# Performance work log

Measured on AMD Instinct MI355X. Metric: run time of the kernel, lower is better.

## Reference

```python
import jax, jax.numpy as jnp
import numpy as np

NEG_SLOPE_GAT = 0.2   # PyG GATConv default negative_slope
NEG_SLOPE = 0.01      # torch.nn.LeakyReLU default
NUM_AISLES = 20       # aisle_nrs drawn from [0,20); matches aisle_nrs.max()+1


def leaky(x, s):
    return jnp.where(x >= 0, x, s * x)


def gat_conv(x, src, dst, W, a_src, a_dst, b, n_nodes):
    """Single-head PyG GATConv (self-loops already appended to src/dst)."""
    h = x @ W                                        # [N, C]
    es = h @ a_src                                   # [N]
    ed = h @ a_dst                                   # [N]
    e = leaky(es[src] + ed[dst], NEG_SLOPE_GAT)      # [E] per-edge score
    m = jax.ops.segment_max(e, dst, num_segments=n_nodes)
    w = jnp.exp(e - m[dst])
    z = jax.ops.segment_sum(w, dst, num_segments=n_nodes)
    alpha = w / z[dst]                               # segment softmax over incoming edges
    out = jax.ops.segment_sum(h[src] * alpha[:, None], dst, num_segments=n_nodes)
    return out + b


def setup_inputs() -> dict:
    key = jax.random.key(0)
    ks = jax.random.split(key, 32)
    B, N, E = 16, 2048, 32768
    Fin, H, O, HA = 32, 128, 64, 256

    def glorot(k, shape):
        fan = shape[0] + shape[-1]
        return jax.random.uniform(k, shape, jnp.float32, -1.0, 1.0) * np.sqrt(6.0 / fan)

    inp = {
        "graph_nodes": jax.random.normal(ks[0], (B, N, Fin), jnp.float32),
        "aisle_nrs": jax.random.randint(ks[1], (B, N), 0, NUM_AISLES),
        "graph_edge_links": jax.random.randint(ks[2], (B, 2, E), 0, N),
        "mask": jax.random.randint(ks[3], (B, N), 0, 2),
        "picks_left": jax.random.randint(ks[4], (B,), 0, 100),
        # GAT layer 1: Fin -> H
        "W1": glorot(ks[5], (Fin, H)), "as1": glorot(ks[6], (H,)), "ad1": glorot(ks[7], (H,)), "b1": jnp.zeros((H,), jnp.float32),
        # GAT layer 2: H -> H
        "W2": glorot(ks[8], (H, H)), "as2": glorot(ks[9], (H,)), "ad2": glorot(ks[10], (H,)), "b2": jnp.zeros((H,), jnp.float32),
        # GAT layer 3: H -> O
        "W3": glorot(ks[11], (H, O)), "as3": glorot(ks[12], (O,)), "ad3": glorot(ks[13], (O,)), "b3": jnp.zeros((O,), jnp.float32),
        # post-embedding MLP head
        "lw1": glorot(ks[14], (2 * O, HA)), "lb1": jnp.zeros((HA,), jnp.float32),
        "lw2": glorot(ks[15], (HA, O)), "lb2": jnp.zeros((O,), jnp.float32),
        "lw3": glorot(ks[16], (O, 1)), "lb3": jnp.zeros((1,), jnp.float32),
    }
    return inp


def reference(graph_nodes, aisle_nrs, graph_edge_links, mask, picks_left,
              W1, as1, ad1, b1, W2, as2, ad2, b2, W3, as3, ad3, b3,
              lw1, lb1, lw2, lb2, lw3, lb3):
    B, N, Fin = graph_nodes.shape
    NT = B * N
    x = graph_nodes.reshape(NT, Fin)

    # batch the graphs: offset per-graph edge indices, append self-loops
    off = (jnp.arange(B) * N)[:, None]
    src = (graph_edge_links[:, 0, :] + off).reshape(-1)
    dst = (graph_edge_links[:, 1, :] + off).reshape(-1)
    loops = jnp.arange(NT)
    src = jnp.concatenate([src, loops])
    dst = jnp.concatenate([dst, loops])

    x = gat_conv(x, src, dst, W1, as1, ad1, b1, NT)
    x = gat_conv(x, src, dst, W2, as2, ad2, b2, NT)
    x = gat_conv(x, src, dst, W3, as3, ad3, b3, NT)

    # scatter-mean aisle embedding
    batch_idx = jnp.repeat(jnp.arange(B), N)
    aid = aisle_nrs.reshape(-1) + batch_idx * NUM_AISLES   # [NT]
    S = B * NUM_AISLES
    ssum = jax.ops.segment_sum(x, aid, num_segments=S)
    cnt = jax.ops.segment_sum(jnp.ones((NT,), x.dtype), aid, num_segments=S)
    emb = ssum / jnp.maximum(cnt, 1.0)[:, None]

    x = jnp.concatenate([x, emb[aid]], axis=1)             # [NT, 2*O]
    x = leaky(x @ lw1 + lb1, NEG_SLOPE)
    x = leaky(x @ lw2 + lb2, NEG_SLOPE)
    x = (x @ lw3 + lb3).reshape(B, N)

    logits = jnp.where(mask != 0, x, -jnp.inf)
    return jax.nn.softmax(logits, axis=1)
```

## Files before the change

kernel.cpp:

```cpp
#include <hip/hip_runtime.h>
#include <hip/hip_bf16.h>
#include <math.h>
#include <stdint.h>

#define BATCH 16
#define NNODE 2048
#define EPG   32768
#define NT    (BATCH * NNODE)
#define ET    (BATCH * EPG + NT)
#define NUM_AISLES 20
#define SEG   (BATCH * NUM_AISLES)
#define NEG_GAT 0.2f
#define NEG_MLP 0.01f
#define ACHUNK 8
#define CAP 64
#define EMB_LD 72

typedef __attribute__((ext_vector_type(8))) short s16x8;
typedef __attribute__((ext_vector_type(4))) float f32x4;

__device__ __forceinline__ void split_bf16(float v, unsigned short& hi, unsigned short& lo) {
    unsigned int u = __float_as_uint(v);
    unsigned int r = u + 0x7FFFu + ((u >> 16) & 1u);
    hi = (unsigned short)(r >> 16);
    float fh = __uint_as_float(((unsigned int)hi) << 16);
    float rem = v - fh;
    unsigned int u2 = __float_as_uint(rem);
    unsigned int r2 = u2 + 0x7FFFu + ((u2 >> 16) & 1u);
    lo = (unsigned short)(r2 >> 16);
}

__device__ __forceinline__ unsigned int pack_bf16(float v) {
    unsigned short h, l;
    split_bf16(v, h, l);
    return ((unsigned int)h << 16) | l;
}

__device__ __forceinline__ float unpack_f32(unsigned int u) {
    return __uint_as_float(u & 0xffff0000u) + __uint_as_float(u << 16);
}

union SU { s16x8 v; unsigned short u[8]; };

__device__ __forceinline__ void unpack_pair(const uint4& u0, const uint4& u1, SU& ah, SU& al) {
    unsigned int uu[8] = {u0.x, u0.y, u0.z, u0.w, u1.x, u1.y, u1.z, u1.w};
#pragma unroll
    for (int j = 0; j < 8; ++j) {
        ah.u[j] = (unsigned short)(uu[j] >> 16);
        al.u[j] = (unsigned short)uu[j];
    }
}

__device__ __forceinline__ void split_pair(const float4& v0, const float4& v1, SU& ah, SU& al) {
    float a8[8] = {v0.x, v0.y, v0.z, v0.w, v1.x, v1.y, v1.z, v1.w};
#pragma unroll
    for (int j = 0; j < 8; ++j) split_bf16(a8[j], ah.u[j], al.u[j]);
}

__device__ __forceinline__ int swz_row0(int bx) {
    int xcd = bx & 7, i = bx >> 3;
    int graph = xcd * 2 + (i >> 5);
    return graph * NNODE + (i & 31) * 64;
}

template <int K, int KC, int NOUT, int COLS>
__device__ __forceinline__ void prep_one(const float* __restrict__ W,
                                         unsigned short* __restrict__ dst, int idx) {
    constexpr int SWM = (KC >= 64) ? 7 : 3;
    int k = idx / NOUT, col = idx - k * NOUT;
    int ch = k / KC, kl = k - ch * KC;
    int ct = col / COLS, n = col - ct * COLS;
    int tile = ct * (K / KC) + ch;
    unsigned short h, l;
    split_bf16(W[idx], h, l);
    size_t base = (size_t)tile * (2 * COLS * KC);
    int pos = n * KC + (kl ^ ((n & SWM) << 3));
    dst[base + pos] = h;
    dst[base + COLS * KC + pos] = l;
}

__global__ __launch_bounds__(256) void prep_weights(const float* __restrict__ W1,
                                                    const float* __restrict__ W2,
                                                    const float* __restrict__ W3,
                                                    const float* __restrict__ lw1,
                                                    const float* __restrict__ lw2,
                                                    unsigned short* __restrict__ P1,
                                                    unsigned short* __restrict__ P2,
                                                    unsigned short* __restrict__ P3,
                                                    unsigned short* __restrict__ P4,
                                                    unsigned short* __restrict__ P5,
                                                    int* __restrict__ cnt,
                                                    int* __restrict__ scount) {
    int b = blockIdx.x, t = threadIdx.x;
    if (b < 16)        prep_one<32, 32, 128, 128>(W1, P1, b * 256 + t);
    else if (b < 80)   prep_one<128, 64, 128, 128>(W2, P2, (b - 16) * 256 + t);
    else if (b < 112)  prep_one<128, 128, 64, 64>(W3, P3, (b - 80) * 256 + t);
    else if (b < 240)  prep_one<128, 64, 256, 128>(lw1, P4, (b - 112) * 256 + t);
    else if (b < 304)  prep_one<256, 128, 64, 64>(lw2, P5, (b - 240) * 256 + t);
    else if (b < 432)  cnt[(b - 304) * 256 + t] = 0;
    else if (t < BATCH) scount[t] = 0;
}

__device__ __forceinline__ void scatter_body(int b, const int* __restrict__ links,
                                             int* __restrict__ cnt,
                                             int* __restrict__ col_bkt) {
    int s, d;
    if (b < 2048) {
        int xcd = b & 7, idx = b >> 3;
        int g = xcd * 2 + (idx >> 7);
        int chunk = idx & 127;
        int i = chunk * 256 + threadIdx.x;
        const int* pb = links + (size_t)g * 2 * EPG;
        s = pb[i] + (g << 11);
        d = pb[EPG + i] + (g << 11);
    } else {
        int b2 = b - 2048;
        int xcd = b2 & 7, idx = b2 >> 3;
        int g = xcd * 2 + (idx >> 3);
        int chunk = idx & 7;
        s = d = g * NNODE + chunk * 256 + threadIdx.x;
    }
    int pos = atomicAdd(&cnt[d], 1);
    if (pos < CAP) col_bkt[d * CAP + pos] = s;
}

template <int K, int KC, int NOUT, int COLS, bool LEAKY, bool ATTN, bool FINAL,
          bool CONCAT, bool PACKEDA, bool PACKOUT>
__device__ __forceinline__ void gemm_body(int bx, int by,
                                          const void* __restrict__ Aptr,
                                          const unsigned short* __restrict__ WP,
                                          const float* __restrict__ bias,
                                          void* __restrict__ outp,
                                          const float* __restrict__ a_src,
                                          const float* __restrict__ a_dst,
                                          float* __restrict__ es,
                                          float* __restrict__ ed,
                                          const float* __restrict__ psum,
                                          const int* __restrict__ pcnt,
                                          const int* __restrict__ aisle,
                                          const float* __restrict__ lw3,
                                          const float* __restrict__ lb3,
                                          const int* __restrict__ mask,
                                          float* __restrict__ logits,
                                          int* __restrict__ scount,
                                          float* __restrict__ smout) {
    constexpr int C = COLS / 16;
    constexpr int SWM = (KC >= 64) ? 7 : 3;
    constexpr int TILE_US = COLS * KC;
    constexpr int TB2 = 2 * TILE_US * 2;
    constexpr int NCH = K / KC;
    constexpr int NKS = KC / 32;
    constexpr int ABYTES = 64 * KC * 4;
    constexpr int SPR = KC / 4;
    constexpr int AROWB = CONCAT ? 256 : K * 4;
    static_assert(TB2 % 4096 == 0, "W chunk must be a multiple of one 256-thread 16B sweep");
    static_assert(ABYTES % 4096 == 0, "A chunk must be a multiple of one 256-thread 16B sweep");
    static_assert(SPR >= 8, "A slot-swizzle needs >=8 slots/row");

    __shared__ unsigned short WS[2 * TILE_US];
    __shared__ unsigned int AS[64 * KC];
    __shared__ float emb_s[CONCAT ? NUM_AISLES * EMB_LD : 1];

    const int tid = threadIdx.x;
    const int wave = tid >> 6, lane = tid & 63;
    const int quad = lane >> 4, l15 = lane & 15;
    const int row0 = swz_row0(bx);
    const int arow = wave * 16 + l15;
    const int m = row0 + arow;

    int am = 0;
    if constexpr (CONCAT) {
        int g = row0 >> 11;
        for (int i = tid; i < NUM_AISLES * 64; i += 256) {
            int a = i >> 6, f = i & 63;
            float s = 0.f;
            int c = 0;
#pragma unroll
            for (int ch = 0; ch < ACHUNK; ++ch) {
                s += psum[((size_t)(g * ACHUNK + ch) * NUM_AISLES + a) * 64 + f];
                c += pcnt[(g * ACHUNK + ch) * NUM_AISLES + a];
            }
            emb_s[a * EMB_LD + f] = s / fmaxf((float)c, 1.0f);
        }
        am = aisle[m];
    }

    f32x4 acc[C];
#pragma unroll
    for (int c = 0; c < C; ++c)
#pragma unroll
        for (int v = 0; v < 4; ++v) acc[c][v] = 0.f;

#pragma unroll
    for (int cidx = 0; cidx < NCH; ++cidx) {
        const char* gsrc = (const char*)WP + (size_t)(by * NCH + cidx) * TB2;
#pragma unroll
        for (int s = 0; s < TB2 / 4096; ++s) {
            __builtin_amdgcn_global_load_lds(
                (const __attribute__((address_space(1))) void*)(gsrc + s * 4096 + wave * 1024 + lane * 16),
                (__attribute__((address_space(3))) void*)&WS[(s * 4096 + wave * 1024) >> 1],
                16, 0, 0);
        }
        if (!CONCAT || cidx == 0) {
#pragma unroll
            for (int s = 0; s < ABYTES / 4096; ++s) {
                int idx16 = s * 256 + tid;
                int row_l = idx16 / SPR;
                int slot = idx16 - row_l * SPR;
                int ssrc = slot ^ (row_l & 7);
                const char* asrc = (const char*)Aptr + (size_t)(row0 + row_l) * AROWB
                                 + (size_t)cidx * KC * 4 + ssrc * 16;
                __builtin_amdgcn_global_load_lds(
                    (const __attribute__((address_space(1))) void*)asrc,
                    (__attribute__((address_space(3))) void*)((char*)AS + (size_t)idx16 * 16),
                    16, 0, 0);
            }
        }
        __syncthreads();

#pragma unroll
        for (int ks = 0; ks < NKS; ++ks) {
            const int t = cidx * NKS + ks;
            SU ah, al;
            if constexpr (CONCAT) {
                if (t < 2) {
                    const char* ab = (const char*)AS + arow * (KC * 4);
                    int slot0 = ks * 8 + quad * 2;
                    uint4 au0 = *(const uint4*)(ab + ((slot0 ^ (arow & 7)) * 16));
                    uint4 au1 = *(const uint4*)(ab + (((slot0 + 1) ^ (arow & 7)) * 16));
                    unpack_pair(au0, au1, ah, al);
                } else {
                    const float* ep = &emb_s[am * EMB_LD + (t * 32 + quad * 8 - 64)];
                    split_pair(((const float4*)ep)[0], ((const float4*)ep)[1], ah, al);
                }
            } else if constexpr (PACKEDA) {
                const char* ab = (const char*)AS + arow * (KC * 4);
                int slot0 = ks * 8 + quad * 2;
                uint4 au0 = *(const uint4*)(ab + ((slot0 ^ (arow & 7)) * 16));
                uint4 au1 = *(const uint4*)(ab + (((slot0 + 1) ^ (arow & 7)) * 16));
                unpack_pair(au0, au1, ah, al);
            } else {
                const char* ab = (const char*)AS + arow * (KC * 4);
                int slot0 = ks * 8 + quad * 2;
                float4 f0 = *(const float4*)(ab + ((slot0 ^ (arow & 7)) * 16));
                float4 f1 = *(const float4*)(ab + (((slot0 + 1) ^ (arow & 7)) * 16));
                split_pair(f0, f1, ah, al);
            }

            const int kq = ks * 32 + quad * 8;
#pragma unroll
            for (int c = 0; c < C; ++c) {
                int n = c * 16 + l15;
                int pos = n * KC + (kq ^ ((n & SWM) << 3));
                s16x8 wh = *(const s16x8*)&WS[pos];
                s16x8 wl = *(const s16x8*)&WS[TILE_US + pos];
                acc[c] = __builtin_amdgcn_mfma_f32_16x16x32_bf16(ah.v, wh, acc[c], 0, 0, 0);
                acc[c] = __builtin_amdgcn_mfma_f32_16x16x32_bf16(ah.v, wl, acc[c], 0, 0, 0);
                acc[c] = __builtin_amdgcn_mfma_f32_16x16x32_bf16(al.v, wh, acc[c], 0, 0, 0);
            }
        }
        if (cidx + 1 < NCH) __syncthreads();
    }
    if constexpr (FINAL) {
        const int g = row0 >> 11;
#pragma unroll
        for (int reg = 0; reg < 4; ++reg) {
            float p = 0.f;
#pragma unroll
            for (int c = 0; c < C; ++c) {
                int colx = c * 16 + l15;
                float v = acc[c][reg] + bias[colx];
                v = v >= 0.f ? v : NEG_MLP * v;
                p += v * lw3[colx];
            }
#pragma unroll
            for (int mk = 1; mk < 16; mk <<= 1) p += __shfl_xor(p, mk, 64);
            if (l15 == 0) {
                int row = row0 + wave * 16 + quad * 4 + reg;
                float lg = p + lb3[0];
                logits[row] = (mask[row] != 0) ? lg : -INFINITY;
            }
        }
        __threadfence();
        __syncthreads();
        __shared__ int slast;
        if (tid == 0) slast = (atomicAdd(&scount[g], 1) == 31) ? 1 : 0;
        __syncthreads();
        if (slast) {
            __threadfence();
            const float* lr = logits + g * NNODE;
            float* op = smout + g * NNODE;
            __shared__ float sred[4], sredz[4];
            float mx = -INFINITY;
            for (int i = tid; i < NNODE; i += 256) mx = fmaxf(mx, lr[i]);
#pragma unroll
            for (int off = 32; off; off >>= 1) mx = fmaxf(mx, __shfl_xor(mx, off, 64));
            if (lane == 0) sred[wave] = mx;
            __syncthreads();
            mx = fmaxf(fmaxf(sred[0], sred[1]), fmaxf(sred[2], sred[3]));
            float z = 0.f;
            for (int i = tid; i < NNODE; i += 256) z += __expf(lr[i] - mx);
#pragma unroll
            for (int off = 32; off; off >>= 1) z += __shfl_xor(z, off, 64);
            if (lane == 0) sredz[wave] = z;
            __syncthreads();
            z = sredz[0] + sredz[1] + sredz[2] + sredz[3];
            float invz = 1.0f / z;
            for (int i = tid; i < NNODE; i += 256) {
                float v = lr[i];
                op[i] = (v == -INFINITY) ? 0.f : __expf(v - mx) * invz;
            }
        }
    } else {
#pragma unroll
        for (int c = 0; c < C; ++c) {
            int colx = by * COLS + c * 16 + l15;
            float bv = bias ? bias[colx] : 0.f;
#pragma unroll
            for (int reg = 0; reg < 4; ++reg) {
                int row = row0 + wave * 16 + quad * 4 + reg;
                float v = acc[c][reg] + bv;
                if (LEAKY) v = v >= 0.f ? v : NEG_MLP * v;
                if constexpr (PACKOUT) {
                    ((unsigned int*)outp)[(size_t)row * NOUT + colx] = pack_bf16(v);
                } else {
                    ((float*)outp)[(size_t)row * NOUT + colx] = v;
                }
            }
        }
        if constexpr (ATTN) {
#pragma unroll
            for (int reg = 0; reg < 4; ++reg) {
                float ps = 0.f, pd = 0.f;
#pragma unroll
                for (int c = 0; c < C; ++c) {
                    int colx = c * 16 + l15;
                    float v = acc[c][reg];
                    ps += v * a_src[colx];
                    pd += v * a_dst[colx];
                }
#pragma unroll
                for (int mk = 1; mk < 16; mk <<= 1) {
                    ps += __shfl_xor(ps, mk, 64);
                    pd += __shfl_xor(pd, mk, 64);
                }
                if (l15 == 0) {
                    int row = row0 + wave * 16 + quad * 4 + reg;
                    es[row] = ps;
                    ed[row] = pd;
                }
            }
        }
    }
}

template <int K, int KC, int NOUT, int COLS, bool LEAKY, bool ATTN, bool FINAL,
          bool CONCAT, bool PACKEDA, bool PACKOUT>
__global__ __launch_bounds__(256) void gemm_mfma(const void* __restrict__ A,
                                                 const unsigned short* __restrict__ WP,
                                                 const float* __restrict__ bias,
                                                 void* __restrict__ out,
                                                 const float* __restrict__ a_src,
                                                 const float* __restrict__ a_dst,
                                                 float* __restrict__ es,
                                                 float* __restrict__ ed,
                                                 const float* __restrict__ psum,
                                                 const int* __restrict__ pcnt,
                                                 const int* __restrict__ aisle,
                                                 const float* __restrict__ lw3,
                                                 const float* __restrict__ lb3,
                                                 const int* __restrict__ mask,
                                                 float* __restrict__ logits,
                                                 int* __restrict__ scount,
                                                 float* __restrict__ smout) {
    gemm_body<K, KC, NOUT, COLS, LEAKY, ATTN, FINAL, CONCAT, PACKEDA, PACKOUT>(
        blockIdx.x, blockIdx.y, A, WP, bias, out, a_src, a_dst, es, ed,
        psum, pcnt, aisle, lw3, lb3, mask, logits, scount, smout);
}

__global__ __launch_bounds__(256) void gemm1_scatter(const float* __restrict__ A,
                                                     const unsigned short* __restrict__ WP,
                                                     float* __restrict__ out,
                                                     const float* __restrict__ a_src,
                                                     const float* __restrict__ a_dst,
                                                     float* __restrict__ es,
                                                     float* __restrict__ ed,
                                                     const int* __restrict__ links,
                                                     int* __restrict__ cnt,
                                                     int* __restrict__ col_bkt) {
    if (blockIdx.x >= NT / 64) {
        scatter_body(blockIdx.x - NT / 64, links, cnt, col_bkt);
        return;
    }
    gemm_body<32, 32, 128, 128, false, true, false, false, false, false>(
        blockIdx.x, 0, A, WP, nullptr, out, a_src, a_dst, es, ed,
        nullptr, nullptr, nullptr, nullptr, nullptr, nullptr, nullptr, nullptr, nullptr);
}

template <int HD>
__global__ __launch_bounds__(256) void gat_aggregate(const float* __restrict__ h,
                                                     const float* __restrict__ es,
                                                     const float* __restrict__ ed,
                                                     const int* __restrict__ cnt,
                                                     const int* __restrict__ col_bkt,
                                                     const float* __restrict__ bias,
                                                     unsigned int* __restrict__ out) {
    int b = blockIdx.x;
    int xcd = b & 7, q = b >> 3;
    int graph = xcd * 2 + (q >> 9);
    int node = graph * NNODE + (q & 511) * 4 + (threadIdx.x >> 6);
    int lane = threadIdx.x & 63;
    int deg = cnt[node];
    deg = deg < CAP ? deg : CAP;
    float edv = ed[node];

    float e0 = -INFINITY;
    int c0v = 0;
    if (lane < deg) {
        c0v = col_bkt[node * CAP + lane];
        float e = es[c0v] + edv;
        e0 = e >= 0.f ? e : NEG_GAT * e;
    }
    float m = e0;
#pragma unroll
    for (int off = 32; off; off >>= 1) m = fmaxf(m, __shfl_xor(m, off, 64));
    float z = __expf(e0 - m);
#pragma unroll
    for (int off = 32; off; off >>= 1) z += __shfl_xor(z, off, 64);
    float w0 = __expf(e0 - m) / z;

    const int quad = lane >> 4, l15 = lane & 15;
    if (HD == 128) {
        float a0 = 0.f, a1 = 0.f, a2 = 0.f, a3 = 0.f;
        float a4 = 0.f, a5 = 0.f, a6 = 0.f, a7 = 0.f;
        for (int jj = 0; jj < deg; jj += 4) {
            int j2 = jj + quad;
            int s = __shfl(c0v, j2, 64);
            float w = __shfl(w0, j2, 64);
            const float* base = h + (size_t)s * 128 + l15 * 8;
            float4 v0 = *(const float4*)base;
            float4 v1 = *(const float4*)(base + 4);
            a0 += w * v0.x; a1 += w * v0.y; a2 += w * v0.z; a3 += w * v0.w;
            a4 += w * v1.x; a5 += w * v1.y; a6 += w * v1.z; a7 += w * v1.w;
        }
#pragma unroll
        for (int off = 16; off <= 32; off <<= 1) {
            a0 += __shfl_xor(a0, off, 64); a1 += __shfl_xor(a1, off, 64);
            a2 += __shfl_xor(a2, off, 64); a3 += __shfl_xor(a3, off, 64);
            a4 += __shfl_xor(a4, off, 64); a5 += __shfl_xor(a5, off, 64);
            a6 += __shfl_xor(a6, off, 64); a7 += __shfl_xor(a7, off, 64);
        }
        if (quad == 0) {
            const float* bb = bias + l15 * 8;
            uint4 p0, p1;
            p0.x = pack_bf16(a0 + bb[0]); p0.y = pack_bf16(a1 + bb[1]);
            p0.z = pack_bf16(a2 + bb[2]); p0.w = pack_bf16(a3 + bb[3]);
            p1.x = pack_bf16(a4 + bb[4]); p1.y = pack_bf16(a5 + bb[5]);
            p1.z = pack_bf16(a6 + bb[6]); p1.w = pack_bf16(a7 + bb[7]);
            unsigned int* op = out + (size_t)node * 128 + l15 * 8;
            *(uint4*)op = p0;
            *(uint4*)(op + 4) = p1;
        }
    } else {
        float a0 = 0.f, a1 = 0.f, a2 = 0.f, a3 = 0.f;
        for (int jj = 0; jj < deg; jj += 4) {
            int j2 = jj + quad;
            int s = __shfl(c0v, j2, 64);
            float w = __shfl(w0, j2, 64);
            float4 v = *(const float4*)(h + (size_t)s * 64 + l15 * 4);
            a0 += w * v.x; a1 += w * v.y; a2 += w * v.z; a3 += w * v.w;
        }
#pragma unroll
        for (int off = 16; off <= 32; off <<= 1) {
            a0 += __shfl_xor(a0, off, 64); a1 += __shfl_xor(a1, off, 64);
            a2 += __shfl_xor(a2, off, 64); a3 += __shfl_xor(a3, off, 64);
        }
        if (quad == 0) {
            const float* bb = bias + l15 * 4;
            uint4 p;
            p.x = pack_bf16(a0 + bb[0]); p.y = pack_bf16(a1 + bb[1]);
            p.z = pack_bf16(a2 + bb[2]); p.w = pack_bf16(a3 + bb[3]);
            *(uint4*)(out + (size_t)node * 64 + l15 * 4) = p;
        }
    }
}

__global__ __launch_bounds__(256) void aisle_partial(const unsigned int* __restrict__ x3,
                                                     const int* __restrict__ aisle,
                                                     float* __restrict__ psum,
                                                     int* __restrict__ pcnt) {
    int xcd = blockIdx.x & 7, idx = blockIdx.x >> 3;
    int g = xcd * 2 + (idx >> 3);
    int ch = idx & 7;
    int pb = g * ACHUNK + ch;
    int f = threadIdx.x & 63;
    int stripe = threadIdx.x >> 6;

    __shared__ float sacc[4][NUM_AISLES][64];
    __shared__ int scnt[4][NUM_AISLES];
    for (int i = threadIdx.x; i < 4 * NUM_AISLES * 64; i += 256)
        ((float*)sacc)[i] = 0.f;
    for (int i = threadIdx.x; i < 4 * NUM_AISLES; i += 256)
        ((int*)scnt)[i] = 0;
    __syncthreads();

    const int* ai = aisle + g * NNODE;
    const unsigned int* xg = x3 + (size_t)g * NNODE * 64;
    int n0 = ch * 256 + stripe * 64;
#pragma unroll 4
    for (int i = 0; i < 64; ++i) {
        int n = n0 + i;
        int a = ai[n];
        float v = unpack_f32(xg[(size_t)n * 64 + f]);
        sacc[stripe][a][f] += v;
        if (f == 0) scnt[stripe][a]++;
    }
    __syncthreads();

    for (int i = threadIdx.x; i < NUM_AISLES * 64; i += 256) {
        int a = i >> 6, ff = i & 63;
        psum[((size_t)pb * NUM_AISLES + a) * 64 + ff] =
            sacc[0][a][ff] + sacc[1][a][ff] + sacc[2][a][ff] + sacc[3][a][ff];
    }
    for (int i = threadIdx.x; i < NUM_AISLES; i += 256) {
        pcnt[pb * NUM_AISLES + i] =
            scnt[0][i] + scnt[1][i] + scnt[2][i] + scnt[3][i];
    }
}


extern "C" void kernel_launch(void* const* d_in, const int* in_sizes, int n_in,
                              void* d_out, int out_size, void* d_ws, size_t ws_size,
                              hipStream_t stream) {
    const float* gn   = (const float*)d_in[0];
    const int* aisle  = (const int*)d_in[1];
    const int* links  = (const int*)d_in[2];
    const int* mask   = (const int*)d_in[3];
    const float* W1  = (const float*)d_in[5];
    const float* as1 = (const float*)d_in[6];
    const float* ad1 = (const float*)d_in[7];
    const float* b1  = (const float*)d_in[8];
    const float* W2  = (const float*)d_in[9];
    const float* as2 = (const float*)d_in[10];
    const float* ad2 = (const float*)d_in[11];
    const float* b2  = (const float*)d_in[12];
    const float* W3  = (const float*)d_in[13];
    const float* as3 = (const float*)d_in[14];
    const float* ad3 = (const float*)d_in[15];
    const float* b3  = (const float*)d_in[16];
    const float* lw1 = (const float*)d_in[17];
    const float* lb1 = (const float*)d_in[18];
    const float* lw2 = (const float*)d_in[19];
    const float* lb2 = (const float*)d_in[20];
    const float* lw3 = (const float*)d_in[21];
    const float* lb3 = (const float*)d_in[22];
    float* out = (float*)d_out;

    float* ws = (float*)d_ws;
    float* h      = ws;
    float* xb     = h + (size_t)NT * 128;
    float* es     = xb + (size_t)NT * 128;
    float* ed     = es + NT;
    float* emb    = ed + NT;
    float* y1     = emb + SEG * 64;
    float* y2     = y1 + (size_t)NT * 256;
    float* logits = y2 + (size_t)NT * 64;
    float* psum   = logits + NT;
    int* pcnt     = (int*)(psum + 128 * NUM_AISLES * 64);
    int* row_ptr  = pcnt + 128 * NUM_AISLES;
    int* cnt      = row_ptr + NT + 1;
    int* scount   = cnt + NT;
    int* col_bkt  = (int*)y2;

    unsigned short* wsplit = (unsigned short*)(((uintptr_t)(scount + BATCH) + 255) & ~(uintptr_t)255);
    unsigned short* P1 = wsplit;
    unsigned short* P2 = P1 + 8192;
    unsigned short* P3 = P2 + 32768;
    unsigned short* P4 = P3 + 16384;
    unsigned short* P5 = P4 + 65536;

    const int EB = (ET + 255) / 256;

    prep_weights<<<433, 256, 0, stream>>>(W1, W2, W3, lw1, lw2, P1, P2, P3, P4, P5, cnt, scount);

    gemm1_scatter<<<NT / 64 + EB, 256, 0, stream>>>(gn, P1, h, as1, ad1, es, ed,
                                                    links, cnt, col_bkt);
    gat_aggregate<128><<<NT / 4, 256, 0, stream>>>(h, es, ed, cnt, col_bkt, b1, (unsigned int*)xb);

    gemm_mfma<128, 64, 128, 128, false, true, false, false, true, false><<<dim3(NT / 64, 1), 256, 0, stream>>>(
        xb, P2, nullptr, h, as2, ad2, es, ed, nullptr, nullptr, nullptr, nullptr, nullptr, nullptr, nullptr, nullptr, nullptr);
    gat_aggregate<128><<<NT / 4, 256, 0, stream>>>(h, es, ed, cnt, col_bkt, b2, (unsigned int*)xb);

    gemm_mfma<128, 128, 64, 64, false, true, false, false, true, false><<<dim3(NT / 64, 1), 256, 0, stream>>>(
        xb, P3, nullptr, h, as3, ad3, es, ed, nullptr, nullptr, nullptr, nullptr, nullptr, nullptr, nullptr, nullptr, nullptr);
    gat_aggregate<64><<<NT / 4, 256, 0, stream>>>(h, es, ed, cnt, col_bkt, b3, (unsigned int*)xb);

    aisle_partial<<<BATCH * ACHUNK, 256, 0, stream>>>((const unsigned int*)xb, aisle, psum, pcnt);

    gemm_mfma<128, 64, 256, 128, true, false, false, true, false, true><<<dim3(NT / 64, 2), 256, 0, stream>>>(
        xb, P4, lb1, y1, nullptr, nullptr, nullptr, nullptr, psum, pcnt, aisle, nullptr, nullptr, nullptr, nullptr, nullptr, nullptr);

    gemm_mfma<256, 128, 64, 64, true, false, true, false, true, false><<<dim3(NT / 64, 1), 256, 0, stream>>>(
        y1, P5, lb2, nullptr, nullptr, nullptr, nullptr, nullptr, nullptr, nullptr, nullptr, lw3, lb3, mask, logits, scount, out);
}
```

Measured before the change: 313.2 us.

## Fuse aisle partial sums into last GAT aggregate via last-block atomic counter

Removes the separate aisle_partial launch. The third gat_aggregate now counts finished blocks per 256-node chunk with an atomic counter, and the last block of each chunk computes that chunk's aisle partial sums and counts. It also shrinks the K-chunk template parameter from 128 to 64 for the W3 and lw2 GEMMs, with matching weight prep. This trades one kernel launch for a threadfence, an extra barrier and an atomic in every aggregate block, plus a serial tail in the last block of each chunk.

```diff
diff --git a/kernel.cpp b/kernel.cpp
--- a/kernel.cpp
+++ b/kernel.cpp
@@ -90,15 +90,19 @@
                                                     unsigned short* __restrict__ P4,
                                                     unsigned short* __restrict__ P5,
                                                     int* __restrict__ cnt,
-                                                    int* __restrict__ scount) {
+                                                    int* __restrict__ scount,
+                                                    int* __restrict__ accnt) {
     int b = blockIdx.x, t = threadIdx.x;
     if (b < 16)        prep_one<32, 32, 128, 128>(W1, P1, b * 256 + t);
     else if (b < 80)   prep_one<128, 64, 128, 128>(W2, P2, (b - 16) * 256 + t);
-    else if (b < 112)  prep_one<128, 128, 64, 64>(W3, P3, (b - 80) * 256 + t);
+    else if (b < 112)  prep_one<128, 64, 64, 64>(W3, P3, (b - 80) * 256 + t);
     else if (b < 240)  prep_one<128, 64, 256, 128>(lw1, P4, (b - 112) * 256 + t);
-    else if (b < 304)  prep_one<256, 128, 64, 64>(lw2, P5, (b - 240) * 256 + t);
+    else if (b < 304)  prep_one<256, 64, 64, 64>(lw2, P5, (b - 240) * 256 + t);
     else if (b < 432)  cnt[(b - 304) * 256 + t] = 0;
-    else if (t < BATCH) scount[t] = 0;
+    else {
+        if (t < BATCH) scount[t] = 0;
+        if (t >= 32 && t < 32 + BATCH * ACHUNK) accnt[t - 32] = 0;
+    }
 }
 
 __device__ __forceinline__ void scatter_body(int b, const int* __restrict__ links,
@@ -397,14 +401,18 @@
         nullptr, nullptr, nullptr, nullptr, nullptr, nullptr, nullptr, nullptr, nullptr);
 }
 
-template <int HD>
+template <int HD, bool FUSEP>
 __global__ __launch_bounds__(256) void gat_aggregate(const float* __restrict__ h,
                                                      const float* __restrict__ es,
                                                      const float* __restrict__ ed,
                                                      const int* __restrict__ cnt,
                                                      const int* __restrict__ col_bkt,
                                                      const float* __restrict__ bias,
-                                                     unsigned int* __restrict__ out) {
+                                                     unsigned int* __restrict__ out,
+                                                     const int* __restrict__ aisle,
+                                                     float* __restrict__ psum,
+                                                     int* __restrict__ pcnt,
+                                                     int* __restrict__ accnt) {
     int b = blockIdx.x;
     int xcd = b & 7, q = b >> 3;
     int graph = xcd * 2 + (q >> 9);
@@ -483,48 +491,48 @@
             *(uint4*)(out + (size_t)node * 64 + l15 * 4) = p;
         }
     }
-}
-
-__global__ __launch_bounds__(256) void aisle_partial(const unsigned int* __restrict__ x3,
-                                                     const int* __restrict__ aisle,
-                                                     float* __restrict__ psum,
-                                                     int* __restrict__ pcnt) {
-    int xcd = blockIdx.x & 7, idx = blockIdx.x >> 3;
-    int g = xcd * 2 + (idx >> 3);
-    int ch = idx & 7;
-    int pb = g * ACHUNK + ch;
-    int f = threadIdx.x & 63;
-    int stripe = threadIdx.x >> 6;
-
-    __shared__ float sacc[4][NUM_AISLES][64];
-    __shared__ int scnt[4][NUM_AISLES];
-    for (int i = threadIdx.x; i < 4 * NUM_AISLES * 64; i += 256)
-        ((float*)sacc)[i] = 0.f;
-    for (int i = threadIdx.x; i < 4 * NUM_AISLES; i += 256)
-        ((int*)scnt)[i] = 0;
-    __syncthreads();
-
-    const int* ai = aisle + g * NNODE;
-    const unsigned int* xg = x3 + (size_t)g * NNODE * 64;
-    int n0 = ch * 256 + stripe * 64;
+
+    if constexpr (FUSEP) {
+        int ch = (q & 511) >> 6;
+        int pb = graph * ACHUNK + ch;
+        __threadfence();
+        __syncthreads();
+        __shared__ int alast;
+        if (threadIdx.x == 0) alast = (atomicAdd(&accnt[pb], 1) == 63) ? 1 : 0;
+        __syncthreads();
+        if (alast) {
+            __threadfence();
+            __shared__ float sacc[4][NUM_AISLES][64];
+            __shared__ int scnt[4][NUM_AISLES];
+            int f = threadIdx.x & 63;
+            int stripe = threadIdx.x >> 6;
+            for (int i = threadIdx.x; i < 4 * NUM_AISLES * 64; i += 256)
+                ((float*)sacc)[i] = 0.f;
+            for (int i = threadIdx.x; i < 4 * NUM_AISLES; i += 256)
+                ((int*)scnt)[i] = 0;
+            __syncthreads();
+            const int* ai = aisle + graph * NNODE;
+            const unsigned int* xg = out + (size_t)graph * NNODE * 64;
+            int n0 = ch * 256 + stripe * 64;
 #pragma unroll 4
-    for (int i = 0; i < 64; ++i) {
-        int n = n0 + i;
-        int a = ai[n];
-        float v = unpack_f32(xg[(size_t)n * 64 + f]);
-        sacc[stripe][a][f] += v;
-        if (f == 0) scnt[stripe][a]++;
-    }
-    __syncthreads();
-
-    for (int i = threadIdx.x; i < NUM_AISLES * 64; i += 256) {
-        int a = i >> 6, ff = i & 63;
-        psum[((size_t)pb * NUM_AISLES + a) * 64 + ff] =
-            sacc[0][a][ff] + sacc[1][a][ff] + sacc[2][a][ff] + sacc[3][a][ff];
-    }
-    for (int i = threadIdx.x; i < NUM_AISLES; i += 256) {
-        pcnt[pb * NUM_AISLES + i] =
-            scnt[0][i] + scnt[1][i] + scnt[2][i] + scnt[3][i];
+            for (int i = 0; i < 64; ++i) {
+                int n = n0 + i;
+                int a = ai[n];
+                float v = unpack_f32(xg[(size_t)n * 64 + f]);
+                sacc[stripe][a][f] += v;
+                if (f == 0) scnt[stripe][a]++;
+            }
+            __syncthreads();
+            for (int i = threadIdx.x; i < NUM_AISLES * 64; i += 256) {
+                int a = i >> 6, ff = i & 63;
+                psum[((size_t)pb * NUM_AISLES + a) * 64 + ff] =
+                    sacc[0][a][ff] + sacc[1][a][ff] + sacc[2][a][ff] + sacc[3][a][ff];
+            }
+            for (int i = threadIdx.x; i < NUM_AISLES; i += 256) {
+                pcnt[pb * NUM_AISLES + i] =
+                    scnt[0][i] + scnt[1][i] + scnt[2][i] + scnt[3][i];
+            }
+        }
     }
 }
 
@@ -570,9 +578,10 @@
     int* row_ptr  = pcnt + 128 * NUM_AISLES;
     int* cnt      = row_ptr + NT + 1;
     int* scount   = cnt + NT;
+    int* accnt    = scount + BATCH;
     int* col_bkt  = (int*)y2;
 
-    unsigned short* wsplit = (unsigned short*)(((uintptr_t)(scount + BATCH) + 255) & ~(uintptr_t)255);
+    unsigned short* wsplit = (unsigned short*)(((uintptr_t)(accnt + BATCH * ACHUNK) + 255) & ~(uintptr_t)255);
     unsigned short* P1 = wsplit;
     unsigned short* P2 = P1 + 8192;
     unsigned short* P3 = P2 + 32768;
@@ -581,25 +590,27 @@
 
     const int EB = (ET + 255) / 256;
 
-    prep_weights<<<433, 256, 0, stream>>>(W1, W2, W3, lw1, lw2, P1, P2, P3, P4, P5, cnt, scount);
+    prep_weights<<<433, 256, 0, stream>>>(W1, W2, W3, lw1, lw2, P1, P2, P3, P4, P5,
+                                          cnt, scount, accnt);
 
     gemm1_scatter<<<NT / 64 + EB, 256, 0, stream>>>(gn, P1, h, as1, ad1, es, ed,
                                                     links, cnt, col_bkt);
-    gat_aggregate<128><<<NT / 4, 256, 0, stream>>>(h, es, ed, cnt, col_bkt, b1, (unsigned int*)xb);
+    gat_aggregate<128, false><<<NT / 4, 256, 0, stream>>>(h, es, ed, cnt, col_bkt, b1,
+        (unsigned int*)xb, nullptr, nullptr, nullptr, nullptr);
 
     gemm_mfma<128, 64, 128, 128, false, true, false, false, true, false><<<dim3(NT / 64, 1), 256, 0, stream>>>(
         xb, P2, nullptr, h, as2, ad2, es, ed, nullptr, nullptr, nullptr, nullptr, nullptr, nullptr, nullptr, nullptr, nullptr);
-    gat_aggregate<128><<<NT / 4, 256, 0, stream>>>(h, es, ed, cnt, col_bkt, b2, (unsigned int*)xb);
-
-    gemm_mfma<128, 128, 64, 64, false, true, false, false, true, false><<<dim3(NT / 64, 1), 256, 0, stream>>>(
+    gat_aggregate<128, false><<<NT / 4, 256, 0, stream>>>(h, es, ed, cnt, col_bkt, b2,
+        (unsigned int*)xb, nullptr, nullptr, nullptr, nullptr);
+
+    gemm_mfma<128, 64, 64, 64, false, true, false, false, true, false><<<dim3(NT / 64, 1), 256, 0, stream>>>(
         xb, P3, nullptr, h, as3, ad3, es, ed, nullptr, nullptr, nullptr, nullptr, nullptr, nullptr, nullptr, nullptr, nullptr);
-    gat_aggregate<64><<<NT / 4, 256, 0, stream>>>(h, es, ed, cnt, col_bkt, b3, (unsigned int*)xb);
-
-    aisle_partial<<<BATCH * ACHUNK, 256, 0, stream>>>((const unsigned int*)xb, aisle, psum, pcnt);
+    gat_aggregate<64, true><<<NT / 4, 256, 0, stream>>>(h, es, ed, cnt, col_bkt, b3,
+        (unsigned int*)xb, aisle, psum, pcnt, accnt);
 
     gemm_mfma<128, 64, 256, 128, true, false, false, true, false, true><<<dim3(NT / 64, 2), 256, 0, stream>>>(
         xb, P4, lb1, y1, nullptr, nullptr, nullptr, nullptr, psum, pcnt, aisle, nullptr, nullptr, nullptr, nullptr, nullptr, nullptr);
 
-    gemm_mfma<256, 128, 64, 64, true, false, true, false, true, false><<<dim3(NT / 64, 1), 256, 0, stream>>>(
+    gemm_mfma<256, 64, 64, 64, true, false, true, false, true, false><<<dim3(NT / 64, 1), 256, 0, stream>>>(
         y1, P5, lb2, nullptr, nullptr, nullptr, nullptr, nullptr, nullptr, nullptr, nullptr, lw3, lb3, mask, logits, scount, out);
 }
```

Result: slower. 894.1 us (+185.4%).
